# Kernel optimization log

Measured on AMD Instinct MI355X. Metric: run time of the kernel, lower is better.

## Reference

```python
import jax, jax.numpy as jnp
import numpy as np

N = 10000   # nodes per type
E = 60000   # edges per edge type
T = 2       # node types (herb, symptom)
H = 8       # heads
F_IN = 2048
HID = 512
OUT = 8
EDGE_TYPES = [(0, 0), (0, 1), (1, 0), (1, 1)]  # (src_type, dst_type) for hh, hs, sh, ss


def segment_softmax(logits, seg, num_segments):
    # logits: [E, H], seg: [E] destination node ids
    m = jax.ops.segment_max(logits, seg, num_segments=num_segments)
    e = jnp.exp(logits - m[seg])
    s = jax.ops.segment_sum(e, seg, num_segments=num_segments)
    return e / (s[seg] + 1e-16)


def hgt_conv(x, edges, Wk, bk, Wq, bq, Wv, bv, Wa, ba, a_rel, m_rel, p_rel):
    # x: [T, N, Fin]; edges: list of 4 int arrays [2, E]
    Fout = Wk.shape[-1]
    D = Fout // H
    k = (jnp.einsum('tnf,tfo->tno', x, Wk) + bk[:, None, :]).reshape(T, N, H, D)
    q = (jnp.einsum('tnf,tfo->tno', x, Wq) + bq[:, None, :]).reshape(T, N, H, D)
    v = (jnp.einsum('tnf,tfo->tno', x, Wv) + bv[:, None, :]).reshape(T, N, H, D)
    inv_sqrt_d = jnp.asarray(1.0 / np.sqrt(D), x.dtype)
    out = jnp.zeros((T, N, H, D), x.dtype)
    for e, (st, dt) in enumerate(EDGE_TYPES):
        src, dst = edges[e][0], edges[e][1]
        k_rel = jnp.einsum('nhd,hde->nhe', k[st], a_rel[e])   # [N,H,D]
        v_rel = jnp.einsum('nhd,hde->nhe', v[st], m_rel[e])
        kj = k_rel[src]          # [E,H,D] gather over source nodes
        vj = v_rel[src]
        qi = q[dt][dst]          # [E,H,D] gather over destination nodes
        alpha = (qi * kj).sum(-1) * p_rel[e] * inv_sqrt_d     # [E,H]
        alpha = segment_softmax(alpha, dst, N)
        agg = jax.ops.segment_sum(vj * alpha[..., None], dst, num_segments=N)
        out = out.at[dt].add(agg)
    out = out.reshape(T, N, Fout)
    out = jnp.einsum('tno,toe->tne', jax.nn.gelu(out, approximate=False), Wa) + ba[:, None, :]
    # HGT skip connection applies only when in_dim == out_dim; never true here (2048->1024->512)
    return out


def setup_inputs() -> dict:
    key = jax.random.key(0)
    ks = jax.random.split(key, 32)
    s = 0.02
    inp = {
        'x': jax.random.normal(ks[0], (T, N, F_IN), jnp.float32),
        'ei_hh': jax.random.randint(ks[1], (2, E), 0, N),
        'ei_hs': jax.random.randint(ks[2], (2, E), 0, N),
        'ei_sh': jax.random.randint(ks[3], (2, E), 0, N),
        'ei_ss': jax.random.randint(ks[4], (2, E), 0, N),
        'Wk1': jax.random.normal(ks[5], (T, F_IN, 2 * HID), jnp.float32) * s,
        'bk1': jnp.zeros((T, 2 * HID), jnp.float32),
        'Wq1': jax.random.normal(ks[6], (T, F_IN, 2 * HID), jnp.float32) * s,
        'bq1': jnp.zeros((T, 2 * HID), jnp.float32),
        'Wv1': jax.random.normal(ks[7], (T, F_IN, 2 * HID), jnp.float32) * s,
        'bv1': jnp.zeros((T, 2 * HID), jnp.float32),
        'Wa1': jax.random.normal(ks[8], (T, 2 * HID, 2 * HID), jnp.float32) * s,
        'ba1': jnp.zeros((T, 2 * HID), jnp.float32),
        'arel1': jax.random.normal(ks[9], (4, H, 128, 128), jnp.float32) * s,
        'mrel1': jax.random.normal(ks[10], (4, H, 128, 128), jnp.float32) * s,
        'prel1': jnp.ones((4, H), jnp.float32),
        'Wk2': jax.random.normal(ks[11], (T, 2 * HID, HID), jnp.float32) * s,
        'bk2': jnp.zeros((T, HID), jnp.float32),
        'Wq2': jax.random.normal(ks[12], (T, 2 * HID, HID), jnp.float32) * s,
        'bq2': jnp.zeros((T, HID), jnp.float32),
        'Wv2': jax.random.normal(ks[13], (T, 2 * HID, HID), jnp.float32) * s,
        'bv2': jnp.zeros((T, HID), jnp.float32),
        'Wa2': jax.random.normal(ks[14], (T, HID, HID), jnp.float32) * s,
        'ba2': jnp.zeros((T, HID), jnp.float32),
        'arel2': jax.random.normal(ks[15], (4, H, 64, 64), jnp.float32) * s,
        'mrel2': jax.random.normal(ks[16], (4, H, 64, 64), jnp.float32) * s,
        'prel2': jnp.ones((4, H), jnp.float32),
        'Wlin': jax.random.normal(ks[17], (HID, OUT), jnp.float32) * s,
        'blin': jnp.zeros((OUT,), jnp.float32),
    }
    return inp


def reference(x, ei_hh, ei_hs, ei_sh, ei_ss,
              Wk1, bk1, Wq1, bq1, Wv1, bv1, Wa1, ba1, arel1, mrel1, prel1,
              Wk2, bk2, Wq2, bq2, Wv2, bv2, Wa2, ba2, arel2, mrel2, prel2,
              Wlin, blin):
    edges = [ei_hh, ei_hs, ei_sh, ei_ss]
    h = hgt_conv(x, edges, Wk1, bk1, Wq1, bq1, Wv1, bv1, Wa1, ba1, arel1, mrel1, prel1)
    h = hgt_conv(h, edges, Wk2, bk2, Wq2, bq2, Wv2, bv2, Wa2, ba2, arel2, mrel2, prel2)
    logits = jnp.einsum('tnf,fo->tno', h, Wlin) + blin   # per-type Linear, then vstack
    return jax.nn.softmax(logits.reshape(T * N, OUT), axis=1)
```

## Files before the change

kernel.cpp:

```cpp
#include <hip/hip_runtime.h>
#include <math.h>

#define NN   10000
#define EE   60000
#define NHEAD 8
#define MPAD 10112

typedef unsigned short ushort_t;
typedef short bf16x8 __attribute__((ext_vector_type(8)));
typedef unsigned short u16x8 __attribute__((ext_vector_type(8)));
typedef unsigned short u16x4 __attribute__((ext_vector_type(4)));
typedef unsigned short u16x2 __attribute__((ext_vector_type(2)));
typedef float floatx4 __attribute__((ext_vector_type(4)));

__device__ __forceinline__ float gelu_f(float x) {
    return 0.5f * x * (1.0f + erff(x * 0.7071067811865476f));
}
__device__ __forceinline__ float bf2f(ushort_t u) {
    union { unsigned i; float f; } v; v.i = ((unsigned)u) << 16; return v.f;
}
__device__ __forceinline__ ushort_t f2bf(float x) {
    unsigned u = __float_as_uint(x);
    u += 0x7fffu + ((u >> 16) & 1u);
    return (ushort_t)(u >> 16);
}
__device__ __forceinline__ void gl_lds16(const void* g, const void* l) {
    __builtin_amdgcn_global_load_lds(
        (const __attribute__((address_space(1))) unsigned int*)(unsigned long long)g,
        (__attribute__((address_space(3))) unsigned int*)(unsigned long long)l,
        16, 0, 0);
}

template<int REL>
__global__ __launch_bounds__(256) void mfma_gemm(
    const ushort_t* __restrict__ A, long Abat, long Abat2, int lda,
    const ushort_t* __restrict__ Bt, long Bbat,
    const float* __restrict__ bias, long bbat,
    ushort_t* __restrict__ C, long Cbat, long Cbat2, int ldc,
    int N, int K)
{
    __shared__ __align__(16) ushort_t As[128 * 32];
    __shared__ __align__(16) ushort_t Bs[128 * 32];
    const int t = threadIdx.x, lane = t & 63, w = t >> 6;
    const int quad = lane >> 4, l15 = lane & 15;
    const int m0 = blockIdx.y * 128, n0 = blockIdx.x * 128;
    const int bz = blockIdx.z;

    long Aoff, Coff;
    const float* bp = nullptr;
    if (REL) {
        const int e = bz >> 3, h = bz & 7;
        Aoff = (long)(e >> 1) * Abat2 + (long)h * N;
        Coff = (long)e * Cbat2 + (long)h * N;
    } else {
        Aoff = (long)bz * Abat;
        Coff = (long)bz * Cbat;
        if (bias) bp = bias + (long)bz * bbat;
    }
    const ushort_t* Ag = A + Aoff + (long)m0 * lda;
    const ushort_t* Bg = Bt + (long)bz * Bbat + (long)n0 * K;
    C += Coff;

    floatx4 acc[4][4];
    #pragma unroll
    for (int i = 0; i < 4; ++i)
        #pragma unroll
        for (int j = 0; j < 4; ++j)
            acc[i][j] = (floatx4){0.f, 0.f, 0.f, 0.f};

    const int wm = (w >> 1) * 64, wn = (w & 1) * 64;
    const int ar0 = t >> 2,         ak0 = (t & 3) * 8;
    const int ar1 = (256 + t) >> 2, ak1 = (t & 3) * 8;
    const char* lA0 = (const char*)As + (size_t)(w * 64) * 16;
    const char* lA1 = (const char*)As + (size_t)(256 + w * 64) * 16;
    const char* lB0 = (const char*)Bs + (size_t)(w * 64) * 16;
    const char* lB1 = (const char*)Bs + (size_t)(256 + w * 64) * 16;

    for (int k0 = 0; k0 < K; k0 += 32) {
        gl_lds16(Ag + (long)ar0 * lda + k0 + ak0, lA0);
        gl_lds16(Ag + (long)ar1 * lda + k0 + ak1, lA1);
        gl_lds16(Bg + (long)ar0 * K + k0 + ak0, lB0);
        gl_lds16(Bg + (long)ar1 * K + k0 + ak1, lB1);
        __syncthreads();
        bf16x8 a[4], b[4];
        #pragma unroll
        for (int mi = 0; mi < 4; ++mi)
            a[mi] = *(const bf16x8*)(As + (size_t)(wm + mi * 16 + l15) * 32 + quad * 8);
        #pragma unroll
        for (int ni = 0; ni < 4; ++ni)
            b[ni] = *(const bf16x8*)(Bs + (size_t)(wn + ni * 16 + l15) * 32 + quad * 8);
        #pragma unroll
        for (int mi = 0; mi < 4; ++mi)
            #pragma unroll
            for (int ni = 0; ni < 4; ++ni)
                acc[mi][ni] = __builtin_amdgcn_mfma_f32_16x16x32_bf16(
                    a[mi], b[ni], acc[mi][ni], 0, 0, 0);
        __syncthreads();
    }

    #pragma unroll
    for (int ni = 0; ni < 4; ++ni) {
        const int col = n0 + wn + ni * 16 + l15;
        if (col >= N) continue;
        const float bv = bp ? bp[col] : 0.f;
        #pragma unroll
        for (int mi = 0; mi < 4; ++mi) {
            const int row = m0 + wm + mi * 16 + quad * 4;
            #pragma unroll
            for (int r = 0; r < 4; ++r)
                C[(long)(row + r) * ldc + col] = f2bf(acc[mi][ni][r] + bv);
        }
    }
}

__global__ void transpose_conv_kernel(
    const float* __restrict__ in, long ibat, int R, int C,
    ushort_t* __restrict__ out, long obat, int Cpad)
{
    __shared__ float tile[32][33];
    in  += (long)blockIdx.z * ibat;
    out += (long)blockIdx.z * obat;
    const int r0 = blockIdx.x * 32, c0 = blockIdx.y * 32;
    const int tx = threadIdx.x, ty = threadIdx.y;
    #pragma unroll
    for (int i = 0; i < 4; ++i) {
        const int r = r0 + ty + i * 8, c = c0 + tx;
        tile[ty + i * 8][tx] = (r < R && c < C) ? in[(long)r * C + c] : 0.f;
    }
    __syncthreads();
    #pragma unroll
    for (int i = 0; i < 4; ++i) {
        const int oc = c0 + ty + i * 8, orr = r0 + tx;
        if (oc < Cpad && orr < R) out[(long)oc * R + orr] = f2bf(tile[tx][ty + i * 8]);
    }
}

__global__ void convpad_kernel(const float* __restrict__ in, ushort_t* __restrict__ out, int logF)
{
    const long per = (long)MPAD << logF;
    const long idx = (long)blockIdx.x * 256 + threadIdx.x;
    if (idx >= per) return;
    const int n = (int)(idx >> logF);
    const int c = (int)(idx & ((1 << logF) - 1));
    const int tt = blockIdx.y;
    float v = 0.f;
    if (n < NN) v = in[(((long)tt * NN + n) << logF) + c];
    out[(long)tt * per + idx] = f2bf(v);
}

__global__ void biascat_kernel(const float* __restrict__ b0, const float* __restrict__ b1,
                               const float* __restrict__ b2, float* __restrict__ out, int F)
{
    const int i = blockIdx.x * 256 + threadIdx.x;
    if (i >= 2 * 3 * F) return;
    const int tt = i / (3 * F), r = i % (3 * F);
    const int sec = r / F, c = r % F;
    const float* b = sec == 0 ? b0 : sec == 1 ? b1 : b2;
    out[i] = b[tt * F + c];
}

__global__ void izero_kernel(int* __restrict__ p, int n) {
    int i = blockIdx.x * 256 + threadIdx.x;
    if (i < n) p[i] = 0;
}

__global__ void hist_kernel(const int* __restrict__ e0, const int* __restrict__ e1,
                            const int* __restrict__ e2, const int* __restrict__ e3,
                            int* __restrict__ counts)
{
    const int i = blockIdx.x * 256 + threadIdx.x;
    if (i >= EE) return;
    const int ty = blockIdx.y;
    const int* ei = ty == 0 ? e0 : ty == 1 ? e1 : ty == 2 ? e2 : e3;
    atomicAdd(&counts[ty * NN + ei[EE + i]], 1);
}

__global__ __launch_bounds__(1024) void scan_kernel(
    const int* __restrict__ counts, int* __restrict__ rowptr, int* __restrict__ wofs)
{
    const int ty = blockIdx.x;
    const int t = threadIdx.x;
    __shared__ int sh[1024];
    __shared__ int carry;
    if (t == 0) carry = 0;
    __syncthreads();
    for (int base = 0; base < NN; base += 1024) {
        const int idx = base + t;
        const int v = (idx < NN) ? counts[ty * NN + idx] : 0;
        sh[t] = v;
        __syncthreads();
        for (int offs = 1; offs < 1024; offs <<= 1) {
            const int add = (t >= offs) ? sh[t - offs] : 0;
            __syncthreads();
            sh[t] += add;
            __syncthreads();
        }
        const int exc = carry + sh[t] - v;
        if (idx < NN) { rowptr[ty * (NN + 1) + idx] = exc; wofs[ty * NN + idx] = exc; }
        __syncthreads();
        if (t == 0) carry += sh[1023];
        __syncthreads();
    }
    if (t == 0) rowptr[ty * (NN + 1) + NN] = carry;
}

__global__ void scatter_kernel(const int* __restrict__ e0, const int* __restrict__ e1,
                               const int* __restrict__ e2, const int* __restrict__ e3,
                               int* __restrict__ wofs, int2* __restrict__ pairs)
{
    const int i = blockIdx.x * 256 + threadIdx.x;
    if (i >= EE) return;
    const int ty = blockIdx.y;
    const int* ei = ty == 0 ? e0 : ty == 1 ? e1 : ty == 2 ? e2 : e3;
    const int src = ei[i], dst = ei[EE + i];
    const int pos = atomicAdd(&wofs[ty * NN + dst], 1);
    pairs[(long)ty * EE + pos] = make_int2(i, src);
}

template<int NV>
__global__ __launch_bounds__(256) void edge_logits_kernel(
    const int* __restrict__ ei, const ushort_t* __restrict__ Qd, int ldq,
    const ushort_t* __restrict__ KR, const float* __restrict__ prel,
    float inv_sqrt_d, float* __restrict__ logit)
{
    const int wave = threadIdx.x >> 6, lane = threadIdx.x & 63;
    const int e = blockIdx.x * 4 + wave;
    if (e >= EE) return;
    const int src = ei[e], dst = ei[EE + e];
    const int HD = NV * 512;
    const ushort_t* q = Qd + (long)dst * ldq + lane * (NV * 8);
    const ushort_t* k = KR + (long)src * HD + lane * (NV * 8);
    float partial = 0.f;
    #pragma unroll
    for (int v = 0; v < NV; ++v) {
        const u16x8 q8 = *(const u16x8*)(q + v * 8);
        const u16x8 k8 = *(const u16x8*)(k + v * 8);
        #pragma unroll
        for (int j = 0; j < 8; ++j)
            partial = fmaf(bf2f(q8[j]), bf2f(k8[j]), partial);
    }
    partial += __shfl_xor(partial, 1);
    partial += __shfl_xor(partial, 2);
    partial += __shfl_xor(partial, 4);
    if ((lane & 7) == 0) {
        const int h = lane >> 3;
        logit[(long)e * 8 + h] = partial * prel[h] * inv_sqrt_d;
    }
}

template<int CPT>
__global__ __launch_bounds__(256) void agg_kernel(
    const int* __restrict__ rp0, const int2* __restrict__ pr0,
    const float* __restrict__ al0, const ushort_t* __restrict__ VR0,
    const int* __restrict__ rp1, const int2* __restrict__ pr1,
    const float* __restrict__ al1, const ushort_t* __restrict__ VR1,
    ushort_t* __restrict__ outp)
{
    const int HD = CPT * 256;
    const int dst = blockIdx.x;
    const int t = threadIdx.x;
    const int c0 = t * CPT;
    if (dst >= NN) {
        if (CPT == 4) *(u16x4*)(outp + (long)dst * HD + c0) = (u16x4){0, 0, 0, 0};
        else          *(u16x2*)(outp + (long)dst * HD + c0) = (u16x2){0, 0};
        return;
    }
    __shared__ float m_s[2][8], si_s[2][8];
    __shared__ int degs[2], starts[2];
    if (t < 2) {
        const int* rp = t ? rp1 : rp0;
        const int a = rp[dst], b = rp[dst + 1];
        starts[t] = a; degs[t] = b - a;
    }
    __syncthreads();
    if (t < 16) {
        const int ty = t >> 3, h = t & 7;
        const int2* pr = ty ? pr1 : pr0;
        const float* al = ty ? al1 : al0;
        const int s0 = starts[ty], dg = degs[ty];
        float m = -3.0e38f;
        for (int i = 0; i < dg; ++i)
            m = fmaxf(m, al[(long)pr[s0 + i].x * 8 + h]);
        float ssum = 0.f;
        for (int i = 0; i < dg; ++i)
            ssum += expf(al[(long)pr[s0 + i].x * 8 + h] - m);
        m_s[ty][h] = m;
        si_s[ty][h] = (dg > 0) ? 1.f / (ssum + 1e-16f) : 0.f;
    }
    __syncthreads();
    const int h = t >> 5;
    float acc[CPT] = {};
    #pragma unroll
    for (int ty = 0; ty < 2; ++ty) {
        const int2* pr = ty ? pr1 : pr0;
        const float* al = ty ? al1 : al0;
        const ushort_t* VR = ty ? VR1 : VR0;
        const int s0 = starts[ty], dg = degs[ty];
        const float mm = m_s[ty][h], si = si_s[ty][h];
        for (int i = 0; i < dg; ++i) {
            const int2 p = pr[s0 + i];
            const float wgt = expf(al[(long)p.x * 8 + h] - mm) * si;
            const ushort_t* vrow = VR + (long)p.y * HD + c0;
            if (CPT == 4) {
                const u16x4 v = *(const u16x4*)vrow;
                #pragma unroll
                for (int j = 0; j < 4; ++j) acc[j] = fmaf(wgt, bf2f(v[j]), acc[j]);
            } else {
                const u16x2 v = *(const u16x2*)vrow;
                #pragma unroll
                for (int j = 0; j < 2; ++j) acc[j] = fmaf(wgt, bf2f(v[j]), acc[j]);
            }
        }
    }
    if (CPT == 4) {
        u16x4 o;
        #pragma unroll
        for (int j = 0; j < 4; ++j) o[j] = f2bf(gelu_f(acc[j]));
        *(u16x4*)(outp + (long)dst * HD + c0) = o;
    } else {
        u16x2 o;
        #pragma unroll
        for (int j = 0; j < 2; ++j) o[j] = f2bf(gelu_f(acc[j]));
        *(u16x2*)(outp + (long)dst * HD + c0) = o;
    }
}

__global__ __launch_bounds__(256) void final_kernel(
    const ushort_t* __restrict__ H2, const float* __restrict__ Wlin,
    const float* __restrict__ blin, float* __restrict__ outp)
{
    const int wave = threadIdx.x >> 6, lane = threadIdx.x & 63;
    const int node = blockIdx.x * 4 + wave;
    if (node >= 2 * NN) return;
    const int tt = (node >= NN) ? 1 : 0;
    const int n = node - tt * NN;
    const ushort_t* hrow = H2 + ((long)tt * MPAD + n) * 512;
    float acc[8] = {};
    for (int f = lane; f < 512; f += 64) {
        const float hv = bf2f(hrow[f]);
        const float* wr = Wlin + f * 8;
        #pragma unroll
        for (int o = 0; o < 8; ++o) acc[o] = fmaf(hv, wr[o], acc[o]);
    }
    #pragma unroll
    for (int o = 0; o < 8; ++o)
        #pragma unroll
        for (int off = 32; off > 0; off >>= 1)
            acc[o] += __shfl_xor(acc[o], off);
    if (lane == 0) {
        float mx = -3.0e38f;
        #pragma unroll
        for (int o = 0; o < 8; ++o) { acc[o] += blin[o]; mx = fmaxf(mx, acc[o]); }
        float ssum = 0.f;
        #pragma unroll
        for (int o = 0; o < 8; ++o) { acc[o] = expf(acc[o] - mx); ssum += acc[o]; }
        const float inv = 1.f / ssum;
        #pragma unroll
        for (int o = 0; o < 8; ++o) outp[(long)node * 8 + o] = acc[o] * inv;
    }
}

static void tconv_launch(const float* in, long ibat, int R, int C,
                         ushort_t* out, long obat, int Cpad, int batch, hipStream_t s)
{
    dim3 grid((R + 31) / 32, (Cpad + 31) / 32, batch);
    transpose_conv_kernel<<<grid, dim3(32, 8), 0, s>>>(in, ibat, R, C, out, obat, Cpad);
}

struct CsrBufs { int *rowptr, *pairs_dummy; int2* pairs; };

static void run_hgt_layer(
    const ushort_t* xb, int Fin, int F,
    const ushort_t* wkqvT, const float* bkqv, const ushort_t* waT, const float* ba,
    const ushort_t* arelT, const ushort_t* mrelT, const float* prel,
    const int* const* ei, const int* rowptr, const int2* pairs,
    ushort_t* kqv, ushort_t* KRall, ushort_t* VRall, float* alpha,
    ushort_t* outg, ushort_t* hout, hipStream_t stream)
{
    const int D = F / NHEAD;
    const float inv_sqrt_d = 1.0f / sqrtf((float)D);
    const long NF = (long)MPAD * F;
    const int ldkqv = 3 * F;

    {
        dim3 grid(3 * F / 128, MPAD / 128, 2);
        mfma_gemm<0><<<grid, 256, 0, stream>>>(
            xb, (long)MPAD * Fin, 0, Fin, wkqvT, (long)3 * F * Fin,
            bkqv, 3 * F, kqv, (long)MPAD * ldkqv, 0, ldkqv, 3 * F, Fin);
    }
    {
        dim3 grid(1, MPAD / 128, 32);
        mfma_gemm<1><<<grid, 256, 0, stream>>>(
            kqv, 0, (long)MPAD * ldkqv, ldkqv, arelT, (long)128 * D,
            nullptr, 0, KRall, 0, NF, F, D, D);
        mfma_gemm<1><<<grid, 256, 0, stream>>>(
            kqv + 2 * F, 0, (long)MPAD * ldkqv, ldkqv, mrelT, (long)128 * D,
            nullptr, 0, VRall, 0, NF, F, D, D);
    }
    for (int e = 0; e < 4; ++e) {
        const int dt = e & 1;
        if (F == 1024)
            edge_logits_kernel<2><<<(EE + 3) / 4, 256, 0, stream>>>(
                ei[e], kqv + (long)dt * MPAD * ldkqv + F, ldkqv,
                KRall + (long)e * NF, prel + e * 8, inv_sqrt_d, alpha + (long)e * EE * 8);
        else
            edge_logits_kernel<1><<<(EE + 3) / 4, 256, 0, stream>>>(
                ei[e], kqv + (long)dt * MPAD * ldkqv + F, ldkqv,
                KRall + (long)e * NF, prel + e * 8, inv_sqrt_d, alpha + (long)e * EE * 8);
    }
    for (int dt = 0; dt < 2; ++dt) {
        const int e0 = dt, e1 = dt + 2;
        if (F == 1024)
            agg_kernel<4><<<MPAD, 256, 0, stream>>>(
                rowptr + e0 * (NN + 1), pairs + (long)e0 * EE, alpha + (long)e0 * EE * 8, VRall + (long)e0 * NF,
                rowptr + e1 * (NN + 1), pairs + (long)e1 * EE, alpha + (long)e1 * EE * 8, VRall + (long)e1 * NF,
                outg + (long)dt * NF);
        else
            agg_kernel<2><<<MPAD, 256, 0, stream>>>(
                rowptr + e0 * (NN + 1), pairs + (long)e0 * EE, alpha + (long)e0 * EE * 8, VRall + (long)e0 * NF,
                rowptr + e1 * (NN + 1), pairs + (long)e1 * EE, alpha + (long)e1 * EE * 8, VRall + (long)e1 * NF,
                outg + (long)dt * NF);
    }
    {
        dim3 grid(F / 128, MPAD / 128, 2);
        mfma_gemm<0><<<grid, 256, 0, stream>>>(
            outg, NF, 0, F, waT, (long)F * F, ba, F, hout, NF, 0, F, F, F);
    }
}

extern "C" void kernel_launch(void* const* d_in, const int* in_sizes, int n_in,
                              void* d_out, int out_size, void* d_ws, size_t ws_size,
                              hipStream_t stream)
{
    const float* x = (const float*)d_in[0];
    const int* ei_arr[4] = {(const int*)d_in[1], (const int*)d_in[2],
                            (const int*)d_in[3], (const int*)d_in[4]};
    const float* Wk1 = (const float*)d_in[5];   const float* bk1 = (const float*)d_in[6];
    const float* Wq1 = (const float*)d_in[7];   const float* bq1 = (const float*)d_in[8];
    const float* Wv1 = (const float*)d_in[9];   const float* bv1 = (const float*)d_in[10];
    const float* Wa1 = (const float*)d_in[11];  const float* ba1 = (const float*)d_in[12];
    const float* ar1 = (const float*)d_in[13];  const float* mr1 = (const float*)d_in[14];
    const float* pr1 = (const float*)d_in[15];
    const float* Wk2 = (const float*)d_in[16];  const float* bk2 = (const float*)d_in[17];
    const float* Wq2 = (const float*)d_in[18];  const float* bq2 = (const float*)d_in[19];
    const float* Wv2 = (const float*)d_in[20];  const float* bv2 = (const float*)d_in[21];
    const float* Wa2 = (const float*)d_in[22];  const float* ba2 = (const float*)d_in[23];
    const float* ar2 = (const float*)d_in[24];  const float* mr2 = (const float*)d_in[25];
    const float* pr2 = (const float*)d_in[26];
    const float* Wlin = (const float*)d_in[27]; const float* blin = (const float*)d_in[28];
    (void)in_sizes; (void)n_in; (void)out_size; (void)ws_size;

    char* base = (char*)d_ws;
    size_t off = 0;
    auto takeF = [&](size_t n) { float* p = (float*)(base + off); off += n * 4; return p; };
    auto takeU = [&](size_t n) { ushort_t* p = (ushort_t*)(base + off);
                                 off += n * 2; off = (off + 15) & ~(size_t)15; return p; };
    auto takeI = [&](size_t n) { int* p = (int*)(base + off); off += n * 4; return p; };

    float* alpha = takeF((size_t)4 * EE * 8);
    float* bkqv1 = takeF((size_t)2 * 3072);
    float* bkqv2 = takeF((size_t)2 * 1536);

    ushort_t* xb     = takeU((size_t)2 * MPAD * 2048);
    ushort_t* kqv    = takeU((size_t)2 * MPAD * 3072);
    ushort_t* KRall  = takeU((size_t)4 * MPAD * 1024);
    ushort_t* VRall  = takeU((size_t)4 * MPAD * 1024);
    ushort_t* outg   = takeU((size_t)2 * MPAD * 1024);
    ushort_t* h1b    = takeU((size_t)2 * MPAD * 1024);
    ushort_t* h2b    = takeU((size_t)2 * MPAD * 512);
    ushort_t* wkqv1t = takeU((size_t)2 * 3072 * 2048);
    ushort_t* wat1   = takeU((size_t)2 * 1024 * 1024);
    ushort_t* wkqv2t = takeU((size_t)2 * 1536 * 1024);
    ushort_t* wat2   = takeU((size_t)2 * 512 * 512);
    ushort_t* ar1t   = takeU((size_t)32 * 128 * 128);
    ushort_t* mr1t   = takeU((size_t)32 * 128 * 128);
    ushort_t* ar2t   = takeU((size_t)32 * 128 * 64);
    ushort_t* mr2t   = takeU((size_t)32 * 128 * 64);

    int*  counts = takeI((size_t)4 * NN);
    int*  wofs   = takeI((size_t)4 * NN);
    int*  rowptr = takeI((size_t)4 * (NN + 1));
    int2* pairs  = (int2*)takeI((size_t)4 * EE * 2);

    {
        const long per = (long)MPAD << 11;
        dim3 grid((unsigned)((per + 255) / 256), 2);
        convpad_kernel<<<grid, 256, 0, stream>>>(x, xb, 11);
    }
    tconv_launch(Wk1, (long)2048 * 1024, 2048, 1024, wkqv1t,                  (long)3072 * 2048, 1024, 2, stream);
    tconv_launch(Wq1, (long)2048 * 1024, 2048, 1024, wkqv1t + (long)1024 * 2048, (long)3072 * 2048, 1024, 2, stream);
    tconv_launch(Wv1, (long)2048 * 1024, 2048, 1024, wkqv1t + (long)2048 * 2048, (long)3072 * 2048, 1024, 2, stream);
    tconv_launch(Wa1, (long)1024 * 1024, 1024, 1024, wat1, (long)1024 * 1024, 1024, 2, stream);
    tconv_launch(Wk2, (long)1024 * 512, 1024, 512, wkqv2t,                   (long)1536 * 1024, 512, 2, stream);
    tconv_launch(Wq2, (long)1024 * 512, 1024, 512, wkqv2t + (long)512 * 1024,  (long)1536 * 1024, 512, 2, stream);
    tconv_launch(Wv2, (long)1024 * 512, 1024, 512, wkqv2t + (long)1024 * 1024, (long)1536 * 1024, 512, 2, stream);
    tconv_launch(Wa2, (long)512 * 512, 512, 512, wat2, (long)512 * 512, 512, 2, stream);
    tconv_launch(ar1, (long)128 * 128, 128, 128, ar1t, (long)128 * 128, 128, 32, stream);
    tconv_launch(mr1, (long)128 * 128, 128, 128, mr1t, (long)128 * 128, 128, 32, stream);
    tconv_launch(ar2, (long)64 * 64, 64, 64, ar2t, (long)128 * 64, 128, 32, stream);
    tconv_launch(mr2, (long)64 * 64, 64, 64, mr2t, (long)128 * 64, 128, 32, stream);
    biascat_kernel<<<(2 * 3072 + 255) / 256, 256, 0, stream>>>(bk1, bq1, bv1, bkqv1, 1024);
    biascat_kernel<<<(2 * 1536 + 255) / 256, 256, 0, stream>>>(bk2, bq2, bv2, bkqv2, 512);

    izero_kernel<<<(4 * NN + 255) / 256, 256, 0, stream>>>(counts, 4 * NN);
    {
        dim3 grid((EE + 255) / 256, 4);
        hist_kernel<<<grid, 256, 0, stream>>>(ei_arr[0], ei_arr[1], ei_arr[2], ei_arr[3], counts);
        scan_kernel<<<4, 1024, 0, stream>>>(counts, rowptr, wofs);
        scatter_kernel<<<grid, 256, 0, stream>>>(ei_arr[0], ei_arr[1], ei_arr[2], ei_arr[3], wofs, pairs);
    }

    run_hgt_layer(xb, 2048, 1024, wkqv1t, bkqv1, wat1, ba1, ar1t, mr1t, pr1,
                  ei_arr, rowptr, pairs, kqv, KRall, VRall, alpha, outg, h1b, stream);
    run_hgt_layer(h1b, 1024, 512, wkqv2t, bkqv2, wat2, ba2, ar2t, mr2t, pr2,
                  ei_arr, rowptr, pairs, kqv, KRall, VRall, alpha, outg, h2b, stream);

    final_kernel<<<(2 * NN + 3) / 4, 256, 0, stream>>>(h2b, Wlin, blin, (float*)d_out);
}
```

Measured before the change: 1.669 ms.

## Pre-swizzle GEMM operands into MFMA tile-blocked layout for contiguous LDS loads

Introduces a tile-blocked swizzled layout (128x32 tiles arranged in MFMA fragment order) for GEMM A and B operands. The producers are changed to write this layout: the input conversion, the weight transposes, the aggregation output and the layer-1 output GEMM. The GEMM can then load each tile with fully contiguous 16-byte global-to-LDS copies and read fragments without strided LDS access. The input conversion is also vectorised to 8-element chunks. This targets uncoalesced global loads and LDS bank conflicts, at the cost of scattered 2-byte stores in swizzled epilogues and more complex index math.

Measured after the change: 1.673 ms. No clear change (+0.2%).

```diff
diff --git a/kernel.cpp b/kernel.cpp
--- a/kernel.cpp
+++ b/kernel.cpp
@@ -30,8 +30,12 @@
         (__attribute__((address_space(3))) unsigned int*)(unsigned long long)l,
         16, 0, 0);
 }
-
-template<int REL>
+__device__ __forceinline__ long swoff(int row, int col, int K) {
+    return ((long)(row >> 7) * (K >> 5) + (col >> 5)) * 4096
+         + (long)(((row & 127) >> 4) * 512 + ((col & 31) >> 3) * 128 + (row & 15) * 8 + (col & 7));
+}
+
+template<int REL, int ASWIZ, int CSWIZ>
 __global__ __launch_bounds__(256) void mfma_gemm(
     const ushort_t* __restrict__ A, long Abat, long Abat2, int lda,
     const ushort_t* __restrict__ Bt, long Bbat,
@@ -57,9 +61,11 @@
         Coff = (long)bz * Cbat;
         if (bias) bp = bias + (long)bz * bbat;
     }
-    const ushort_t* Ag = A + Aoff + (long)m0 * lda;
-    const ushort_t* Bg = Bt + (long)bz * Bbat + (long)n0 * K;
     C += Coff;
+
+    const ushort_t* Ags = ASWIZ ? A + Aoff + (long)(m0 >> 7) * (K >> 5) * 4096
+                                : A + Aoff + (long)m0 * lda;
+    const ushort_t* Bgs = Bt + (long)bz * Bbat + (long)(n0 >> 7) * (K >> 5) * 4096;
 
     floatx4 acc[4][4];
     #pragma unroll
@@ -68,7 +74,6 @@
         for (int j = 0; j < 4; ++j)
             acc[i][j] = (floatx4){0.f, 0.f, 0.f, 0.f};
 
-    const int wm = (w >> 1) * 64, wn = (w & 1) * 64;
     const int ar0 = t >> 2,         ak0 = (t & 3) * 8;
     const int ar1 = (256 + t) >> 2, ak1 = (t & 3) * 8;
     const char* lA0 = (const char*)As + (size_t)(w * 64) * 16;
@@ -76,19 +81,33 @@
     const char* lB0 = (const char*)Bs + (size_t)(w * 64) * 16;
     const char* lB1 = (const char*)Bs + (size_t)(256 + w * 64) * 16;
 
+    const int wm = (w >> 1) * 64, wn = (w & 1) * 64;
+    const int pa = (w >> 1) * 4, pb = (w & 1) * 4;
+
     for (int k0 = 0; k0 < K; k0 += 32) {
-        gl_lds16(Ag + (long)ar0 * lda + k0 + ak0, lA0);
-        gl_lds16(Ag + (long)ar1 * lda + k0 + ak1, lA1);
-        gl_lds16(Bg + (long)ar0 * K + k0 + ak0, lB0);
-        gl_lds16(Bg + (long)ar1 * K + k0 + ak1, lB1);
+        if (ASWIZ) {
+            const ushort_t* ab = Ags + (size_t)(k0 >> 5) * 4096;
+            gl_lds16(ab + (size_t)(w * 64 + lane) * 8, lA0);
+            gl_lds16(ab + (size_t)(256 + w * 64 + lane) * 8, lA1);
+        } else {
+            gl_lds16(Ags + (long)ar0 * lda + k0 + ak0, lA0);
+            gl_lds16(Ags + (long)ar1 * lda + k0 + ak1, lA1);
+        }
+        const ushort_t* bb = Bgs + (size_t)(k0 >> 5) * 4096;
+        gl_lds16(bb + (size_t)(w * 64 + lane) * 8, lB0);
+        gl_lds16(bb + (size_t)(256 + w * 64 + lane) * 8, lB1);
         __syncthreads();
         bf16x8 a[4], b[4];
         #pragma unroll
-        for (int mi = 0; mi < 4; ++mi)
-            a[mi] = *(const bf16x8*)(As + (size_t)(wm + mi * 16 + l15) * 32 + quad * 8);
+        for (int mi = 0; mi < 4; ++mi) {
+            if (ASWIZ)
+                a[mi] = *(const bf16x8*)(As + (size_t)((pa + mi) * 64 + lane) * 8);
+            else
+                a[mi] = *(const bf16x8*)(As + (size_t)(wm + mi * 16 + l15) * 32 + quad * 8);
+        }
         #pragma unroll
         for (int ni = 0; ni < 4; ++ni)
-            b[ni] = *(const bf16x8*)(Bs + (size_t)(wn + ni * 16 + l15) * 32 + quad * 8);
+            b[ni] = *(const bf16x8*)(Bs + (size_t)((pb + ni) * 64 + lane) * 8);
         #pragma unroll
         for (int mi = 0; mi < 4; ++mi)
             #pragma unroll
@@ -107,8 +126,11 @@
         for (int mi = 0; mi < 4; ++mi) {
             const int row = m0 + wm + mi * 16 + quad * 4;
             #pragma unroll
-            for (int r = 0; r < 4; ++r)
-                C[(long)(row + r) * ldc + col] = f2bf(acc[mi][ni][r] + bv);
+            for (int r = 0; r < 4; ++r) {
+                const float v = acc[mi][ni][r] + bv;
+                if (CSWIZ) C[swoff(row + r, col, ldc)] = f2bf(v);
+                else       C[(long)(row + r) * ldc + col] = f2bf(v);
+            }
         }
     }
 }
@@ -131,21 +153,34 @@
     #pragma unroll
     for (int i = 0; i < 4; ++i) {
         const int oc = c0 + ty + i * 8, orr = r0 + tx;
-        if (oc < Cpad && orr < R) out[(long)oc * R + orr] = f2bf(tile[tx][ty + i * 8]);
+        if (oc < Cpad && orr < R)
+            out[swoff(oc, orr, R)] = f2bf(tile[tx][ty + i * 8]);
     }
 }
 
 __global__ void convpad_kernel(const float* __restrict__ in, ushort_t* __restrict__ out, int logF)
 {
-    const long per = (long)MPAD << logF;
-    const long idx = (long)blockIdx.x * 256 + threadIdx.x;
-    if (idx >= per) return;
-    const int n = (int)(idx >> logF);
-    const int c = (int)(idx & ((1 << logF) - 1));
+    const long chunks = ((long)MPAD << logF) >> 3;
+    const long cid = (long)blockIdx.x * 256 + threadIdx.x;
+    if (cid >= chunks) return;
     const int tt = blockIdx.y;
-    float v = 0.f;
-    if (n < NN) v = in[(((long)tt * NN + n) << logF) + c];
-    out[(long)tt * per + idx] = f2bf(v);
+    const int ksh = logF - 5;
+    const long tile = cid >> 9;
+    const int  c9 = (int)(cid & 511);
+    const int  it = (int)(tile >> ksh);
+    const int  kk = (int)(tile & ((1 << ksh) - 1));
+    const int  p = c9 >> 6, q = (c9 >> 4) & 3, r = c9 & 15;
+    const int  row = it * 128 + p * 16 + r;
+    const int  col = kk * 32 + q * 8;
+    u16x8 o = (u16x8){0, 0, 0, 0, 0, 0, 0, 0};
+    if (row < NN) {
+        const float* src = in + (((long)tt * NN + row) << logF) + col;
+        const float4 a = *(const float4*)src;
+        const float4 b = *(const float4*)(src + 4);
+        o[0] = f2bf(a.x); o[1] = f2bf(a.y); o[2] = f2bf(a.z); o[3] = f2bf(a.w);
+        o[4] = f2bf(b.x); o[5] = f2bf(b.y); o[6] = f2bf(b.z); o[7] = f2bf(b.w);
+    }
+    *(u16x8*)(out + (((long)tt * MPAD) << logF) + cid * 8) = o;
 }
 
 __global__ void biascat_kernel(const float* __restrict__ b0, const float* __restrict__ b1,
@@ -260,9 +295,10 @@
     const int dst = blockIdx.x;
     const int t = threadIdx.x;
     const int c0 = t * CPT;
+    const long oofs = swoff(dst, c0, HD);
     if (dst >= NN) {
-        if (CPT == 4) *(u16x4*)(outp + (long)dst * HD + c0) = (u16x4){0, 0, 0, 0};
-        else          *(u16x2*)(outp + (long)dst * HD + c0) = (u16x2){0, 0};
+        if (CPT == 4) *(u16x4*)(outp + oofs) = (u16x4){0, 0, 0, 0};
+        else          *(u16x2*)(outp + oofs) = (u16x2){0, 0};
         return;
     }
     __shared__ float m_s[2][8], si_s[2][8];
@@ -316,12 +352,12 @@
         u16x4 o;
         #pragma unroll
         for (int j = 0; j < 4; ++j) o[j] = f2bf(gelu_f(acc[j]));
-        *(u16x4*)(outp + (long)dst * HD + c0) = o;
+        *(u16x4*)(outp + oofs) = o;
     } else {
         u16x2 o;
         #pragma unroll
         for (int j = 0; j < 2; ++j) o[j] = f2bf(gelu_f(acc[j]));
-        *(u16x2*)(outp + (long)dst * HD + c0) = o;
+        *(u16x2*)(outp + oofs) = o;
     }
 }
 
@@ -367,10 +403,8 @@
     transpose_conv_kernel<<<grid, dim3(32, 8), 0, s>>>(in, ibat, R, C, out, obat, Cpad);
 }
 
-struct CsrBufs { int *rowptr, *pairs_dummy; int2* pairs; };
-
 static void run_hgt_layer(
-    const ushort_t* xb, int Fin, int F,
+    const ushort_t* xb, int Fin, int F, int swout,
     const ushort_t* wkqvT, const float* bkqv, const ushort_t* waT, const float* ba,
     const ushort_t* arelT, const ushort_t* mrelT, const float* prel,
     const int* const* ei, const int* rowptr, const int2* pairs,
@@ -384,16 +418,16 @@
 
     {
         dim3 grid(3 * F / 128, MPAD / 128, 2);
-        mfma_gemm<0><<<grid, 256, 0, stream>>>(
+        mfma_gemm<0, 1, 0><<<grid, 256, 0, stream>>>(
             xb, (long)MPAD * Fin, 0, Fin, wkqvT, (long)3 * F * Fin,
             bkqv, 3 * F, kqv, (long)MPAD * ldkqv, 0, ldkqv, 3 * F, Fin);
     }
     {
         dim3 grid(1, MPAD / 128, 32);
-        mfma_gemm<1><<<grid, 256, 0, stream>>>(
+        mfma_gemm<1, 0, 0><<<grid, 256, 0, stream>>>(
             kqv, 0, (long)MPAD * ldkqv, ldkqv, arelT, (long)128 * D,
             nullptr, 0, KRall, 0, NF, F, D, D);
-        mfma_gemm<1><<<grid, 256, 0, stream>>>(
+        mfma_gemm<1, 0, 0><<<grid, 256, 0, stream>>>(
             kqv + 2 * F, 0, (long)MPAD * ldkqv, ldkqv, mrelT, (long)128 * D,
             nullptr, 0, VRall, 0, NF, F, D, D);
     }
@@ -423,8 +457,12 @@
     }
     {
         dim3 grid(F / 128, MPAD / 128, 2);
-        mfma_gemm<0><<<grid, 256, 0, stream>>>(
-            outg, NF, 0, F, waT, (long)F * F, ba, F, hout, NF, 0, F, F, F);
+        if (swout)
+            mfma_gemm<0, 1, 1><<<grid, 256, 0, stream>>>(
+                outg, NF, 0, F, waT, (long)F * F, ba, F, hout, NF, 0, F, F, F);
+        else
+            mfma_gemm<0, 1, 0><<<grid, 256, 0, stream>>>(
+                outg, NF, 0, F, waT, (long)F * F, ba, F, hout, NF, 0, F, F, F);
     }
 }
 
@@ -483,15 +521,14 @@
     int2* pairs  = (int2*)takeI((size_t)4 * EE * 2);
 
     {
-        const long per = (long)MPAD << 11;
-        dim3 grid((unsigned)((per + 255) / 256), 2);
-        convpad_kernel<<<grid, 256, 0, stream>>>(x, xb, 11);
-    }
-    tconv_launch(Wk1, (long)2048 * 1024, 2048, 1024, wkqv1t,                  (long)3072 * 2048, 1024, 2, stream);
+        dim3 grid((unsigned)((((long)MPAD << 11) >> 3 + 0) / 256 + ((((long)MPAD << 11) >> 3) % 256 ? 1 : 0)), 2);
+        convpad_kernel<<<dim3(MPAD, 2), 256, 0, stream>>>(x, xb, 11);
+    }
+    tconv_launch(Wk1, (long)2048 * 1024, 2048, 1024, wkqv1t,                     (long)3072 * 2048, 1024, 2, stream);
     tconv_launch(Wq1, (long)2048 * 1024, 2048, 1024, wkqv1t + (long)1024 * 2048, (long)3072 * 2048, 1024, 2, stream);
     tconv_launch(Wv1, (long)2048 * 1024, 2048, 1024, wkqv1t + (long)2048 * 2048, (long)3072 * 2048, 1024, 2, stream);
     tconv_launch(Wa1, (long)1024 * 1024, 1024, 1024, wat1, (long)1024 * 1024, 1024, 2, stream);
-    tconv_launch(Wk2, (long)1024 * 512, 1024, 512, wkqv2t,                   (long)1536 * 1024, 512, 2, stream);
+    tconv_launch(Wk2, (long)1024 * 512, 1024, 512, wkqv2t,                     (long)1536 * 1024, 512, 2, stream);
     tconv_launch(Wq2, (long)1024 * 512, 1024, 512, wkqv2t + (long)512 * 1024,  (long)1536 * 1024, 512, 2, stream);
     tconv_launch(Wv2, (long)1024 * 512, 1024, 512, wkqv2t + (long)1024 * 1024, (long)1536 * 1024, 512, 2, stream);
     tconv_launch(Wa2, (long)512 * 512, 512, 512, wat2, (long)512 * 512, 512, 2, stream);
@@ -510,9 +547,9 @@
         scatter_kernel<<<grid, 256, 0, stream>>>(ei_arr[0], ei_arr[1], ei_arr[2], ei_arr[3], wofs, pairs);
     }
 
-    run_hgt_layer(xb, 2048, 1024, wkqv1t, bkqv1, wat1, ba1, ar1t, mr1t, pr1,
+    run_hgt_layer(xb, 2048, 1024, 1, wkqv1t, bkqv1, wat1, ba1, ar1t, mr1t, pr1,
                   ei_arr, rowptr, pairs, kqv, KRall, VRall, alpha, outg, h1b, stream);
-    run_hgt_layer(h1b, 1024, 512, wkqv2t, bkqv2, wat2, ba2, ar2t, mr2t, pr2,
+    run_hgt_layer(h1b, 1024, 512, 0, wkqv2t, bkqv2, wat2, ba2, ar2t, mr2t, pr2,
                   ei_arr, rowptr, pairs, kqv, KRall, VRall, alpha, outg, h2b, stream);
 
     final_kernel<<<(2 * NN + 3) / 4, 256, 0, stream>>>(h2b, Wlin, blin, (float*)d_out);
```
